# Optimization experiments

Measured on AMD Instinct MI355X. Metric: run time of the kernel, lower is better.

Reference implementation:

```python
import jax, jax.numpy as jnp
import numpy as np

N, E, F_IN, H, H2, G, C = 30000, 480000, 1280, 512, 256, 64, 10


def _linear_init(key, fan_in, fan_out):
    k1, k2 = jax.random.split(key)
    s = 1.0 / np.sqrt(fan_in)
    W = jax.random.uniform(k1, (fan_in, fan_out), jnp.float32, -s, s)
    b = jax.random.uniform(k2, (fan_out,), jnp.float32, -s, s)
    return W, b


def setup_inputs() -> dict:
    key = jax.random.key(0)
    ks = jax.random.split(key, 6)
    x = jax.random.normal(ks[0], (N, F_IN), jnp.float32)
    edge_index = jax.random.randint(ks[1], (2, E), 0, N, dtype=jnp.int32).astype(jnp.int64)
    batch = jnp.sort(jax.random.randint(ks[2], (N,), 0, G, dtype=jnp.int32)).astype(jnp.int64)
    W1, b1 = _linear_init(ks[3], F_IN, H)
    beta2 = jnp.ones((), jnp.float32)  # AGNNConv beta init = 1.0 (trainable in prop2)
    W2, b2 = _linear_init(ks[4], H, H2)
    W3, b3 = _linear_init(ks[5], 2 * H2, C)
    return {"x": x, "edge_index": edge_index, "batch": batch,
            "W1": W1, "b1": b1, "beta2": beta2,
            "W2": W2, "b2": b2, "W3": W3, "b3": b3}


def _agnn(x, src, dst, beta, n):
    # L2 normalize (PyG F.normalize: clamp norm at 1e-12)
    norm = jnp.maximum(jnp.linalg.norm(x, axis=-1, keepdims=True), 1e-12)
    xn = x / norm
    # per-edge cosine similarity attention logits
    alpha = beta * jnp.sum(xn[src] * xn[dst], axis=-1)  # [E']
    # softmax over incoming edges of each destination node
    amax = jax.ops.segment_max(alpha, dst, num_segments=n)
    ex = jnp.exp(alpha - amax[dst])
    denom = jax.ops.segment_sum(ex, dst, num_segments=n)
    w = ex / denom[dst]
    # weighted scatter-add of raw source features
    return jax.ops.segment_sum(w[:, None] * x[src], dst, num_segments=n)


def reference(x, edge_index, batch, W1, b1, beta2, W2, b2, W3, b3):
    n = x.shape[0]
    h = jax.nn.relu(x @ W1 + b1)  # [N, 512]
    # AGNNConv adds self-loops by default
    loops = jnp.arange(n, dtype=edge_index.dtype)
    src = jnp.concatenate([edge_index[0], loops])
    dst = jnp.concatenate([edge_index[1], loops])
    h = _agnn(h, src, dst, jnp.float32(1.0), n)  # prop1: fixed beta=1
    h = _agnn(h, src, dst, beta2, n)             # prop2: learned beta
    h = jax.nn.relu(h @ W2 + b2)  # [N, 256]
    # global max / mean pool per graph
    gmx = jax.ops.segment_max(h, batch, num_segments=G)
    cnt = jnp.maximum(jax.ops.segment_sum(jnp.ones((n,), h.dtype), batch, num_segments=G), 1.0)
    gav = jax.ops.segment_sum(h, batch, num_segments=G) / cnt[:, None]
    return jnp.concatenate([gmx, gav], axis=1) @ W3 + b3  # [G, C]
```

## Files before the change

### kernel.cpp

```cpp
#include <hip/hip_runtime.h>
#include <hip/hip_bf16.h>
#include <cstdint>


typedef __attribute__((ext_vector_type(8))) short bf16x8;
typedef __attribute__((ext_vector_type(4))) float f32x4;
typedef __attribute__((ext_vector_type(8))) unsigned short ushort8;
typedef __attribute__((ext_vector_type(4))) unsigned short ushort4v;
typedef __attribute__((ext_vector_type(4))) unsigned int uint4v;

__device__ inline unsigned short f2bf(float f) {
    unsigned int u = __float_as_uint(f);
    u += 0x7FFFu + ((u >> 16) & 1u);
    return (unsigned short)(u >> 16);
}

__device__ __forceinline__ float bf2f(unsigned short u) {
    return __uint_as_float(((unsigned int)u) << 16);
}

__device__ __forceinline__ unsigned int cvtpk(float lo, float hi) {
    unsigned int r;
    asm("v_cvt_pk_bf16_f32 %0, %1, %2" : "=v"(r) : "v"(lo), "v"(hi));
    return r;
}

__device__ __forceinline__ void gload_lds16(const void* g, void* l) {
    __builtin_amdgcn_global_load_lds(
        (const __attribute__((address_space(1))) void*)g,
        (__attribute__((address_space(3))) void*)l, 16, 0, 0);
}

__device__ __forceinline__ float wave_sum_dpp(float p) {
    int t;
    t = __builtin_amdgcn_update_dpp(0, __float_as_int(p), 0xB1, 0xf, 0xf, true);
    p += __int_as_float(t);
    t = __builtin_amdgcn_update_dpp(0, __float_as_int(p), 0x4E, 0xf, 0xf, true);
    p += __int_as_float(t);
    t = __builtin_amdgcn_update_dpp(0, __float_as_int(p), 0x141, 0xf, 0xf, true);
    p += __int_as_float(t);
    t = __builtin_amdgcn_update_dpp(0, __float_as_int(p), 0x140, 0xf, 0xf, true);
    p += __int_as_float(t);
    t = __builtin_amdgcn_update_dpp(0, __float_as_int(p), 0x142, 0xf, 0xf, true);
    p += __int_as_float(t);
    t = __builtin_amdgcn_update_dpp(0, __float_as_int(p), 0x143, 0xf, 0xf, true);
    p += __int_as_float(t);
    return __int_as_float(__builtin_amdgcn_readlane(__float_as_int(p), 63));
}

__global__ __launch_bounds__(256) void k_transpose_bf16(
    const float* __restrict__ W, unsigned short* __restrict__ Wt, int K, int N) {
    __shared__ unsigned short t[32][33];
    int k0 = blockIdx.x * 32, n0 = blockIdx.y * 32;
    int tr = threadIdx.x >> 3;
    int tc = (threadIdx.x & 7) * 4;
    float4 v = *(const float4*)(W + (long)(k0 + tr) * N + n0 + tc);
    t[tr][tc + 0] = f2bf(v.x); t[tr][tc + 1] = f2bf(v.y);
    t[tr][tc + 2] = f2bf(v.z); t[tr][tc + 3] = f2bf(v.w);
    __syncthreads();
    ushort4v o = { t[tc + 0][tr], t[tc + 1][tr], t[tc + 2][tr], t[tc + 3][tr] };
    *(ushort4v*)(Wt + (long)(n0 + tr) * K + k0 + tc) = o;
}

template <int K, int BN, int NOUT, bool AF32, bool OUTBF16>
__global__ __launch_bounds__(512, 4) void k_gemm_bias_relu(
    const void* __restrict__ Av, const unsigned short* __restrict__ Bt,
    const float* __restrict__ bias, void* __restrict__ Cv, int M) {
    constexpr int NSTEP = K / 32;
    __shared__ unsigned short As[2][128 * 32];
    __shared__ unsigned short Bs[2][BN * 32];
    int tid = threadIdx.x;
    int w = tid >> 6, l = tid & 63;
    int wm = w >> 2, wn = w & 3;
    int mBase = blockIdx.x * 128;
    int nBase = blockIdx.y * BN;

    const float* Af = (const float*)Av;
    const unsigned short* Ab = (const unsigned short*)Av;

    int arow = tid >> 2;
    int aslot = (tid & 3) ^ ((arow >> 1) & 3);
    long aRowG = mBase + arow; if (aRowG >= M) aRowG = M - 1;
    const float* aptr = AF32 ? (Af + aRowG * K + (tid & 3) * 8) : nullptr;

    auto stageB = [&](int b, int k0) {
#pragma unroll
        for (int o = 0; o < BN / 128; ++o) {
            int rbase = (w * (BN / 128) + o) * 16;
            int row = rbase + (l >> 2);
            int gsrc = (l & 3) ^ ((row >> 1) & 3);
            gload_lds16(Bt + (long)(nBase + row) * K + k0 + gsrc * 8,
                        &Bs[b][rbase * 32]);
        }
    };
    auto stageAbf = [&](int b, int k0) {
        int rbase = w * 16;
        int row = rbase + (l >> 2);
        int gsrc = (l & 3) ^ ((row >> 1) & 3);
        long gr = mBase + row; if (gr >= M) gr = M - 1;
        gload_lds16(Ab + gr * K + k0 + gsrc * 8, &As[b][rbase * 32]);
    };

    f32x4 acc[4][4] = {};
    float4 Aw0 = {}, Aw1 = {}, An0 = {}, An1 = {};

    stageB(0, 0);
    if constexpr (AF32) {
        float4 z0 = *(const float4*)(aptr);
        float4 z1 = *(const float4*)(aptr + 4);
        uint4v p = { cvtpk(z0.x, z0.y), cvtpk(z0.z, z0.w),
                     cvtpk(z1.x, z1.y), cvtpk(z1.z, z1.w) };
        *(uint4v*)(&As[0][arow * 32 + aslot * 8]) = p;
        if (NSTEP > 1) {
            Aw0 = *(const float4*)(aptr + 32);
            Aw1 = *(const float4*)(aptr + 36);
        }
    } else {
        stageAbf(0, 0);
    }
    __syncthreads();

    int s = 0;
    for (int step = 0; step < NSTEP; ++step, s ^= 1) {
        int nk = (step + 1) * 32;
        int nk2 = (step + 2) * 32;
        if (nk < K) {
            stageB(s ^ 1, nk);
            if constexpr (!AF32) stageAbf(s ^ 1, nk);
        }
        if constexpr (AF32) {
            if (nk2 < K) {
                An0 = *(const float4*)(aptr + nk2);
                An1 = *(const float4*)(aptr + nk2 + 4);
            }
        }
        bf16x8 af[4];
#pragma unroll
        for (int m = 0; m < 4; ++m) {
            int ra = wm * 64 + m * 16 + (l & 15);
            int g = (l >> 4) ^ ((ra >> 1) & 3);
            af[m] = *(const bf16x8*)(&As[s][ra * 32 + g * 8]);
        }
#pragma unroll
        for (int n = 0; n < 4; ++n) {
            int rb = wn * 64 + n * 16 + (l & 15);
            int g = (l >> 4) ^ ((rb >> 1) & 3);
            bf16x8 bfr = *(const bf16x8*)(&Bs[s][rb * 32 + g * 8]);
#pragma unroll
            for (int m = 0; m < 4; ++m)
                acc[m][n] = __builtin_amdgcn_mfma_f32_16x16x32_bf16(
                    af[m], bfr, acc[m][n], 0, 0, 0);
        }
        if constexpr (AF32) {
            if (nk < K) {
                uint4v p = { cvtpk(Aw0.x, Aw0.y), cvtpk(Aw0.z, Aw0.w),
                             cvtpk(Aw1.x, Aw1.y), cvtpk(Aw1.z, Aw1.w) };
                *(uint4v*)(&As[s ^ 1][arow * 32 + aslot * 8]) = p;
                Aw0 = An0; Aw1 = An1;
            }
        }
        __syncthreads();
    }

#pragma unroll
    for (int m = 0; m < 4; ++m) {
        int row = mBase + wm * 64 + m * 16 + (l >> 4) * 4;
#pragma unroll
        for (int n = 0; n < 4; ++n) {
            int colg = nBase + wn * 64 + n * 16 + (l & 15);
            float bv = bias[colg];
#pragma unroll
            for (int r = 0; r < 4; ++r) {
                if (row + r < M) {
                    float v = fmaxf(acc[m][n][r] + bv, 0.f);
                    if constexpr (OUTBF16)
                        ((unsigned short*)Cv)[(long)(row + r) * NOUT + colg] = f2bf(v);
                    else
                        ((float*)Cv)[(long)(row + r) * NOUT + colg] = v;
                }
            }
        }
    }
}

__global__ void k_csr_init(int* __restrict__ cnt, int* __restrict__ fill, int n) {
    int i = blockIdx.x * blockDim.x + threadIdx.x;
    if (i < n) { cnt[i] = 1; fill[i] = 0; }
}

__global__ void k_csr_count(const int* __restrict__ ei, int* __restrict__ cnt, int E) {
    int e = blockIdx.x * blockDim.x + threadIdx.x;
    if (e < E) atomicAdd(&cnt[ei[E + e]], 1);
}

__global__ __launch_bounds__(1024) void k_scan1(const int* __restrict__ cnt,
                                                int* __restrict__ rowp,
                                                int* __restrict__ bsum, int n) {
    __shared__ int wsum[16];
    int b = blockIdx.x, t = threadIdx.x, lane = t & 63, w = t >> 6;
    int i = b * 1024 + t;
    int v = (i < n) ? cnt[i] : 0;
    int x = v;
#pragma unroll
    for (int off = 1; off < 64; off <<= 1) {
        int y = __shfl_up(x, off, 64);
        if (lane >= off) x += y;
    }
    if (lane == 63) wsum[w] = x;
    __syncthreads();
    if (t < 16) {
        int s = wsum[t];
#pragma unroll
        for (int off = 1; off < 16; off <<= 1) {
            int y = __shfl_up(s, off, 64);
            if (t >= off) s += y;
        }
        wsum[t] = s;
    }
    __syncthreads();
    int wo = w ? wsum[w - 1] : 0;
    if (i < n) rowp[i] = wo + x - v;
    if (t == 0) bsum[b] = wsum[15];
}

__global__ __launch_bounds__(64) void k_scan2(int* __restrict__ bsum, int nb) {
    int lane = threadIdx.x;
    int v = (lane < nb) ? bsum[lane] : 0;
    int x = v;
#pragma unroll
    for (int off = 1; off < 64; off <<= 1) {
        int y = __shfl_up(x, off, 64);
        if (lane >= off) x += y;
    }
    int total = __shfl(x, nb - 1, 64);
    if (lane < nb) bsum[lane] = x - v;
    if (lane == 0) bsum[nb] = total;
}

__global__ __launch_bounds__(1024) void k_scan3(const int* __restrict__ bsum,
                                                int* __restrict__ rowp, int n, int nb) {
    int i = blockIdx.x * 1024 + threadIdx.x;
    if (i < n) rowp[i] += bsum[i >> 10];
    else if (i == n) rowp[n] = bsum[nb];
}

__global__ void k_csr_fill(const int* __restrict__ ei, const int* __restrict__ rowp,
                           int* __restrict__ fill, int* __restrict__ col, int E, int n) {
    int idx = blockIdx.x * blockDim.x + threadIdx.x;
    if (idx < E) {
        int d = ei[E + idx];
        int s = ei[idx];
        int pos = atomicAdd(&fill[d], 1);
        col[rowp[d] + pos] = s;
    } else if (idx < E + n) {
        int nd = idx - E;
        int pos = atomicAdd(&fill[nd], 1);
        col[rowp[nd] + pos] = nd;
    }
}

__global__ __launch_bounds__(256) void k_norm_bf16(const unsigned short* __restrict__ h,
                                                   float* __restrict__ invn, int n) {
    int row = blockIdx.x * 4 + (threadIdx.x >> 6);
    int lane = threadIdx.x & 63;
    if (row >= n) return;
    ushort8 v = *(const ushort8*)(h + (long)row * 512 + lane * 8);
    float s = 0.f;
#pragma unroll
    for (int e = 0; e < 8; ++e) { float f = bf2f(v[e]); s += f * f; }
    s = wave_sum_dpp(s);
    if (lane == 0) invn[row] = 1.f / fmaxf(sqrtf(s), 1e-12f);
}

__global__ __launch_bounds__(256) void k_agnn(
    const unsigned short* __restrict__ h, const float* __restrict__ invn,
    const int* __restrict__ rowp, const int* __restrict__ col,
    const float* __restrict__ beta_ptr, unsigned short* __restrict__ out,
    float* __restrict__ invn_out, int nNodes) {
    int dst = blockIdx.x * 4 + (threadIdx.x >> 6);
    int lane = threadIdx.x & 63;
    if (dst >= nNodes) return;
    float beta = beta_ptr ? beta_ptr[0] : 1.0f;
    ushort8 hdv = *(const ushort8*)(h + (long)dst * 512 + lane * 8);
    float hd[8];
#pragma unroll
    for (int e = 0; e < 8; ++e) hd[e] = bf2f(hdv[e]);
    float coef = beta * invn[dst];
    float mshift = fabsf(beta) * 1.0625f;
    int s0 = rowp[dst], s1 = rowp[dst + 1];

    float ssum = 0.f;
    float accE[8] = {0.f, 0.f, 0.f, 0.f, 0.f, 0.f, 0.f, 0.f};
    float accO[8] = {0.f, 0.f, 0.f, 0.f, 0.f, 0.f, 0.f, 0.f};

    for (int base = s0; base < s1; base += 64) {
        int cnt = min(s1 - base, 64);
        int gi = base + lane; if (gi >= s1) gi = s1 - 1;
        int idxl = col[gi];
        float vinl = invn[idxl];
        ushort8 r0 = {}, r1 = {}, r2 = {}, r3 = {};
        r0 = *(const ushort8*)(h + (long)__builtin_amdgcn_readlane(idxl, 0) * 512 + lane * 8);
        if (cnt > 1) r1 = *(const ushort8*)(h + (long)__builtin_amdgcn_readlane(idxl, 1) * 512 + lane * 8);
        if (cnt > 2) r2 = *(const ushort8*)(h + (long)__builtin_amdgcn_readlane(idxl, 2) * 512 + lane * 8);
        if (cnt > 3) r3 = *(const ushort8*)(h + (long)__builtin_amdgcn_readlane(idxl, 3) * 512 + lane * 8);
        int j = 0;
        for (; j + 1 < cnt; j += 2) {
            ushort8 c0 = r0, c1 = r1;
            r0 = r2; r1 = r3;
            if (j + 4 < cnt) r2 = *(const ushort8*)(h + (long)__builtin_amdgcn_readlane(idxl, j + 4) * 512 + lane * 8);
            if (j + 5 < cnt) r3 = *(const ushort8*)(h + (long)__builtin_amdgcn_readlane(idxl, j + 5) * 512 + lane * 8);
            float a0[8], a1[8];
#pragma unroll
            for (int e = 0; e < 8; ++e) { a0[e] = bf2f(c0[e]); a1[e] = bf2f(c1[e]); }
            float p0 = a0[0] * hd[0] + a0[1] * hd[1] + a0[2] * hd[2] + a0[3] * hd[3] +
                       a0[4] * hd[4] + a0[5] * hd[5] + a0[6] * hd[6] + a0[7] * hd[7];
            float p1 = a1[0] * hd[0] + a1[1] * hd[1] + a1[2] * hd[2] + a1[3] * hd[3] +
                       a1[4] * hd[4] + a1[5] * hd[5] + a1[6] * hd[6] + a1[7] * hd[7];
            p0 = wave_sum_dpp(p0);
            p1 = wave_sum_dpp(p1);
            float al0 = coef * __int_as_float(__builtin_amdgcn_readlane(__float_as_int(vinl), j)) * p0;
            float al1 = coef * __int_as_float(__builtin_amdgcn_readlane(__float_as_int(vinl), j + 1)) * p1;
            float w0 = __expf(al0 - mshift);
            float w1 = __expf(al1 - mshift);
            ssum += w0 + w1;
#pragma unroll
            for (int e = 0; e < 8; ++e) { accE[e] += w0 * a0[e]; accO[e] += w1 * a1[e]; }
        }
        if (j < cnt) {
            float a0[8];
#pragma unroll
            for (int e = 0; e < 8; ++e) a0[e] = bf2f(r0[e]);
            float p0 = a0[0] * hd[0] + a0[1] * hd[1] + a0[2] * hd[2] + a0[3] * hd[3] +
                       a0[4] * hd[4] + a0[5] * hd[5] + a0[6] * hd[6] + a0[7] * hd[7];
            p0 = wave_sum_dpp(p0);
            float al0 = coef * __int_as_float(__builtin_amdgcn_readlane(__float_as_int(vinl), j)) * p0;
            float w0 = __expf(al0 - mshift);
            ssum += w0;
#pragma unroll
            for (int e = 0; e < 8; ++e) accE[e] += w0 * a0[e];
        }
    }
    float inv_s = 1.f / ssum;
    float acc[8];
#pragma unroll
    for (int e = 0; e < 8; ++e) acc[e] = (accE[e] + accO[e]) * inv_s;

    uint4v o = { cvtpk(acc[0], acc[1]), cvtpk(acc[2], acc[3]),
                 cvtpk(acc[4], acc[5]), cvtpk(acc[6], acc[7]) };
    *(uint4v*)(out + (long)dst * 512 + lane * 8) = o;

    if (invn_out) {
        float s = 0.f;
#pragma unroll
        for (int e = 0; e < 8; ++e) s += acc[e] * acc[e];
        s = wave_sum_dpp(s);
        if (lane == 0) invn_out[dst] = 1.f / fmaxf(sqrtf(s), 1e-12f);
    }
}

__global__ void k_bounds(const int* __restrict__ batch, int* __restrict__ starts,
                         int n, int G) {
    int g = blockIdx.x * blockDim.x + threadIdx.x;
    if (g > G) return;
    int lo = 0, hi = n;
    while (lo < hi) {
        int mid = (lo + hi) >> 1;
        if (batch[mid] < g) lo = mid + 1; else hi = mid;
    }
    starts[g] = lo;
}

__global__ __launch_bounds__(256) void k_pool(const float* __restrict__ h3,
                                              const int* __restrict__ starts,
                                              float* __restrict__ pooled) {
    int g = blockIdx.x;
    int t = threadIdx.x;
    int s = starts[g], e = starts[g + 1];
    float mx = -3.402823466e38f, sm = 0.f;
    int r = s;
    for (; r + 4 <= e; r += 4) {
        float v0 = h3[(long)(r + 0) * 256 + t];
        float v1 = h3[(long)(r + 1) * 256 + t];
        float v2 = h3[(long)(r + 2) * 256 + t];
        float v3 = h3[(long)(r + 3) * 256 + t];
        mx = fmaxf(mx, fmaxf(fmaxf(v0, v1), fmaxf(v2, v3)));
        sm += (v0 + v1) + (v2 + v3);
    }
    for (; r < e; ++r) {
        float v = h3[(long)r * 256 + t];
        mx = fmaxf(mx, v); sm += v;
    }
    float cnt = fmaxf((float)(e - s), 1.f);
    pooled[g * 512 + t] = mx;
    pooled[g * 512 + 256 + t] = sm / cnt;
}

__global__ __launch_bounds__(64) void k_final(const float* __restrict__ pooled,
                                              const float* __restrict__ W3,
                                              const float* __restrict__ b3,
                                              float* __restrict__ out, int C) {
    int g = blockIdx.x;
    int lane = threadIdx.x;
    for (int c = 0; c < C; c++) {
        float p = 0.f;
        for (int k = lane; k < 512; k += 64) p += pooled[g * 512 + k] * W3[k * C + c];
#pragma unroll
        for (int off = 32; off; off >>= 1) p += __shfl_xor(p, off, 64);
        if (lane == 0) out[g * C + c] = p + b3[c];
    }
}

extern "C" void kernel_launch(void* const* d_in, const int* in_sizes, int n_in,
                              void* d_out, int out_size, void* d_ws, size_t ws_size,
                              hipStream_t stream) {
    const float* x     = (const float*)d_in[0];
    const int*   ei    = (const int*)d_in[1];
    const int*   batch = (const int*)d_in[2];
    const float* W1    = (const float*)d_in[3];
    const float* b1    = (const float*)d_in[4];
    const float* beta2 = (const float*)d_in[5];
    const float* W2    = (const float*)d_in[6];
    const float* b2    = (const float*)d_in[7];
    const float* W3    = (const float*)d_in[8];
    const float* b3    = (const float*)d_in[9];
    float* out = (float*)d_out;

    const int N = in_sizes[2];
    const int E = in_sizes[1] / 2;
    const int F_IN = in_sizes[0] / N;
    const int H = in_sizes[4];
    const int H2 = in_sizes[7];
    const int C = in_sizes[9];
    const int G = out_size / C;

    char* ws = (char*)d_ws;
    unsigned short* H1B = (unsigned short*)(ws + 0);
    unsigned short* HPB = (unsigned short*)(ws + 31000000L);
    unsigned short* H2B = (unsigned short*)(ws + 62000000L);
    float*          H3  = (float*)(ws + 0);
    unsigned short* W1T = (unsigned short*)(ws + 93000000L);
    unsigned short* W2T = (unsigned short*)(ws + 94500000L);
    float* INVN_A = (float*)(ws + 95000000L);
    float* INVN_B = (float*)(ws + 95200000L);
    int*   CNT    = (int*)(ws + 95400000L);
    int*   FILL   = (int*)(ws + 95600000L);
    int*   ROWP   = (int*)(ws + 95800000L);
    int*   COL    = (int*)(ws + 96000000L);
    int*   BSUM   = (int*)(ws + 98100000L);
    int*   START  = (int*)(ws + 98110000L);
    float* POOLED = (float*)(ws + 98120000L);

    { dim3 g1(F_IN / 32, H / 32); k_transpose_bf16<<<g1, 256, 0, stream>>>(W1, W1T, F_IN, H); }
    { dim3 g2(H / 32, H2 / 32);   k_transpose_bf16<<<g2, 256, 0, stream>>>(W2, W2T, H, H2); }

    int nb = (N + 1023) / 1024;
    k_csr_init<<<(N + 255) / 256, 256, 0, stream>>>(CNT, FILL, N);
    k_csr_count<<<(E + 255) / 256, 256, 0, stream>>>(ei, CNT, E);
    k_scan1<<<nb, 1024, 0, stream>>>(CNT, ROWP, BSUM, N);
    k_scan2<<<1, 64, 0, stream>>>(BSUM, nb);
    k_scan3<<<(N + 1 + 1023) / 1024, 1024, 0, stream>>>(BSUM, ROWP, N, nb);
    k_csr_fill<<<(E + N + 255) / 256, 256, 0, stream>>>(ei, ROWP, FILL, COL, E, N);

    {
        dim3 grid((N + 127) / 128, H / 256);
        k_gemm_bias_relu<1280, 256, 512, true, true>
            <<<grid, 512, 0, stream>>>(x, W1T, b1, H1B, N);
    }

    k_norm_bf16<<<(N + 3) / 4, 256, 0, stream>>>(H1B, INVN_A, N);
    k_agnn<<<(N + 3) / 4, 256, 0, stream>>>(H1B, INVN_A, ROWP, COL, nullptr, HPB, INVN_B, N);

    k_agnn<<<(N + 3) / 4, 256, 0, stream>>>(HPB, INVN_B, ROWP, COL, beta2, H2B, nullptr, N);

    {
        dim3 grid((N + 127) / 128, 1);
        k_gemm_bias_relu<512, 256, 256, false, false>
            <<<grid, 512, 0, stream>>>(H2B, W2T, b2, H3, N);
    }

    k_bounds<<<1, 128, 0, stream>>>(batch, START, N, G);
    k_pool<<<G, 256, 0, stream>>>(H3, START, POOLED);
    k_final<<<G, 64, 0, stream>>>(POOLED, W3, b3, out, C);
}
```

Measured before the change: 379.3 us.

## Merge small launches, shrink GEMM2 tile, emit bf16 H3, and simplify A prefetch

Fuses the two weight-transpose kernels into one launch, merges scan2 and scan3 into one kernel, and folds the batch-bounds search into the pooling kernel, which cuts three launches. The second GEMM now uses BN=128 with two column blocks, so it launches more workgroups, and it writes its output as bf16 to halve the bytes the pooling kernel reads. The fp32 A prefetch in the first GEMM now runs one step ahead instead of two, which may expose more load latency. Storing H3 as bf16 adds rounding error before pooling.

```diff
diff --git a/kernel.cpp b/kernel.cpp
--- a/kernel.cpp
+++ b/kernel.cpp
@@ -48,17 +48,30 @@
     return __int_as_float(__builtin_amdgcn_readlane(__float_as_int(p), 63));
 }
 
-__global__ __launch_bounds__(256) void k_transpose_bf16(
-    const float* __restrict__ W, unsigned short* __restrict__ Wt, int K, int N) {
-    __shared__ unsigned short t[32][33];
-    int k0 = blockIdx.x * 32, n0 = blockIdx.y * 32;
+__global__ __launch_bounds__(256) void k_transpose_both(
+    const float* __restrict__ W1, unsigned short* __restrict__ W1T,
+    int K1, int N1, int nt1,
+    const float* __restrict__ W2, unsigned short* __restrict__ W2T,
+    int K2, int N2) {
+    __shared__ unsigned short tb[32][33];
+    int id = blockIdx.x;
+    const float* W; unsigned short* Wt; int K, N, bx, by;
+    if (id < nt1) {
+        W = W1; Wt = W1T; K = K1; N = N1;
+        int nx = K1 / 32; bx = id % nx; by = id / nx;
+    } else {
+        id -= nt1;
+        W = W2; Wt = W2T; K = K2; N = N2;
+        int nx = K2 / 32; bx = id % nx; by = id / nx;
+    }
+    int k0 = bx * 32, n0 = by * 32;
     int tr = threadIdx.x >> 3;
     int tc = (threadIdx.x & 7) * 4;
     float4 v = *(const float4*)(W + (long)(k0 + tr) * N + n0 + tc);
-    t[tr][tc + 0] = f2bf(v.x); t[tr][tc + 1] = f2bf(v.y);
-    t[tr][tc + 2] = f2bf(v.z); t[tr][tc + 3] = f2bf(v.w);
-    __syncthreads();
-    ushort4v o = { t[tc + 0][tr], t[tc + 1][tr], t[tc + 2][tr], t[tc + 3][tr] };
+    tb[tr][tc + 0] = f2bf(v.x); tb[tr][tc + 1] = f2bf(v.y);
+    tb[tr][tc + 2] = f2bf(v.z); tb[tr][tc + 3] = f2bf(v.w);
+    __syncthreads();
+    ushort4v o = { tb[tc + 0][tr], tb[tc + 1][tr], tb[tc + 2][tr], tb[tc + 3][tr] };
     *(ushort4v*)(Wt + (long)(n0 + tr) * K + k0 + tc) = o;
 }
 
@@ -67,6 +80,7 @@
     const void* __restrict__ Av, const unsigned short* __restrict__ Bt,
     const float* __restrict__ bias, void* __restrict__ Cv, int M) {
     constexpr int NSTEP = K / 32;
+    constexpr int NF = BN / 64;
     __shared__ unsigned short As[2][128 * 32];
     __shared__ unsigned short Bs[2][BN * 32];
     int tid = threadIdx.x;
@@ -101,8 +115,7 @@
         gload_lds16(Ab + gr * K + k0 + gsrc * 8, &As[b][rbase * 32]);
     };
 
-    f32x4 acc[4][4] = {};
-    float4 Aw0 = {}, Aw1 = {}, An0 = {}, An1 = {};
+    f32x4 acc[4][NF] = {};
 
     stageB(0, 0);
     if constexpr (AF32) {
@@ -111,10 +124,6 @@
         uint4v p = { cvtpk(z0.x, z0.y), cvtpk(z0.z, z0.w),
                      cvtpk(z1.x, z1.y), cvtpk(z1.z, z1.w) };
         *(uint4v*)(&As[0][arow * 32 + aslot * 8]) = p;
-        if (NSTEP > 1) {
-            Aw0 = *(const float4*)(aptr + 32);
-            Aw1 = *(const float4*)(aptr + 36);
-        }
     } else {
         stageAbf(0, 0);
     }
@@ -123,15 +132,14 @@
     int s = 0;
     for (int step = 0; step < NSTEP; ++step, s ^= 1) {
         int nk = (step + 1) * 32;
-        int nk2 = (step + 2) * 32;
+        float4 f0, f1;
         if (nk < K) {
             stageB(s ^ 1, nk);
-            if constexpr (!AF32) stageAbf(s ^ 1, nk);
-        }
-        if constexpr (AF32) {
-            if (nk2 < K) {
-                An0 = *(const float4*)(aptr + nk2);
-                An1 = *(const float4*)(aptr + nk2 + 4);
+            if constexpr (AF32) {
+                f0 = *(const float4*)(aptr + nk);
+                f1 = *(const float4*)(aptr + nk + 4);
+            } else {
+                stageAbf(s ^ 1, nk);
             }
         }
         bf16x8 af[4];
@@ -142,8 +150,8 @@
             af[m] = *(const bf16x8*)(&As[s][ra * 32 + g * 8]);
         }
 #pragma unroll
-        for (int n = 0; n < 4; ++n) {
-            int rb = wn * 64 + n * 16 + (l & 15);
+        for (int n = 0; n < NF; ++n) {
+            int rb = wn * (BN / 4) + n * 16 + (l & 15);
             int g = (l >> 4) ^ ((rb >> 1) & 3);
             bf16x8 bfr = *(const bf16x8*)(&Bs[s][rb * 32 + g * 8]);
 #pragma unroll
@@ -153,10 +161,9 @@
         }
         if constexpr (AF32) {
             if (nk < K) {
-                uint4v p = { cvtpk(Aw0.x, Aw0.y), cvtpk(Aw0.z, Aw0.w),
-                             cvtpk(Aw1.x, Aw1.y), cvtpk(Aw1.z, Aw1.w) };
+                uint4v p = { cvtpk(f0.x, f0.y), cvtpk(f0.z, f0.w),
+                             cvtpk(f1.x, f1.y), cvtpk(f1.z, f1.w) };
                 *(uint4v*)(&As[s ^ 1][arow * 32 + aslot * 8]) = p;
-                Aw0 = An0; Aw1 = An1;
             }
         }
         __syncthreads();
@@ -166,8 +173,8 @@
     for (int m = 0; m < 4; ++m) {
         int row = mBase + wm * 64 + m * 16 + (l >> 4) * 4;
 #pragma unroll
-        for (int n = 0; n < 4; ++n) {
-            int colg = nBase + wn * 64 + n * 16 + (l & 15);
+        for (int n = 0; n < NF; ++n) {
+            int colg = nBase + wn * (BN / 4) + n * 16 + (l & 15);
             float bv = bias[colg];
 #pragma unroll
             for (int r = 0; r < 4; ++r) {
@@ -223,25 +230,25 @@
     if (t == 0) bsum[b] = wsum[15];
 }
 
-__global__ __launch_bounds__(64) void k_scan2(int* __restrict__ bsum, int nb) {
-    int lane = threadIdx.x;
-    int v = (lane < nb) ? bsum[lane] : 0;
-    int x = v;
-#pragma unroll
-    for (int off = 1; off < 64; off <<= 1) {
-        int y = __shfl_up(x, off, 64);
-        if (lane >= off) x += y;
-    }
-    int total = __shfl(x, nb - 1, 64);
-    if (lane < nb) bsum[lane] = x - v;
-    if (lane == 0) bsum[nb] = total;
-}
-
-__global__ __launch_bounds__(1024) void k_scan3(const int* __restrict__ bsum,
-                                                int* __restrict__ rowp, int n, int nb) {
-    int i = blockIdx.x * 1024 + threadIdx.x;
-    if (i < n) rowp[i] += bsum[i >> 10];
-    else if (i == n) rowp[n] = bsum[nb];
+__global__ __launch_bounds__(1024) void k_scan23(const int* __restrict__ bsum,
+                                                 int* __restrict__ rowp, int n, int nb) {
+    __shared__ int off[65];
+    int t = threadIdx.x;
+    if (t < 64) {
+        int v = (t < nb) ? bsum[t] : 0;
+        int x = v;
+#pragma unroll
+        for (int o = 1; o < 64; o <<= 1) {
+            int y = __shfl_up(x, o, 64);
+            if (t >= o) x += y;
+        }
+        off[t] = x - v;
+        if (t == nb - 1) off[64] = x;
+    }
+    __syncthreads();
+    int i = blockIdx.x * 1024 + t;
+    if (i < n) rowp[i] += off[i >> 10];
+    else if (i == n) rowp[n] = off[64];
 }
 
 __global__ void k_csr_fill(const int* __restrict__ ei, const int* __restrict__ rowp,
@@ -358,36 +365,35 @@
     }
 }
 
-__global__ void k_bounds(const int* __restrict__ batch, int* __restrict__ starts,
-                         int n, int G) {
-    int g = blockIdx.x * blockDim.x + threadIdx.x;
-    if (g > G) return;
-    int lo = 0, hi = n;
-    while (lo < hi) {
-        int mid = (lo + hi) >> 1;
-        if (batch[mid] < g) lo = mid + 1; else hi = mid;
-    }
-    starts[g] = lo;
-}
-
-__global__ __launch_bounds__(256) void k_pool(const float* __restrict__ h3,
-                                              const int* __restrict__ starts,
-                                              float* __restrict__ pooled) {
+__global__ __launch_bounds__(256) void k_pool(const unsigned short* __restrict__ h3,
+                                              const int* __restrict__ batch,
+                                              float* __restrict__ pooled, int n) {
+    __shared__ int se[2];
     int g = blockIdx.x;
+    if (threadIdx.x < 2) {
+        int tgt = g + (int)threadIdx.x;
+        int lo = 0, hi = n;
+        while (lo < hi) {
+            int mid = (lo + hi) >> 1;
+            if (batch[mid] < tgt) lo = mid + 1; else hi = mid;
+        }
+        se[threadIdx.x] = lo;
+    }
+    __syncthreads();
+    int s = se[0], e = se[1];
     int t = threadIdx.x;
-    int s = starts[g], e = starts[g + 1];
     float mx = -3.402823466e38f, sm = 0.f;
     int r = s;
     for (; r + 4 <= e; r += 4) {
-        float v0 = h3[(long)(r + 0) * 256 + t];
-        float v1 = h3[(long)(r + 1) * 256 + t];
-        float v2 = h3[(long)(r + 2) * 256 + t];
-        float v3 = h3[(long)(r + 3) * 256 + t];
+        float v0 = bf2f(h3[(long)(r + 0) * 256 + t]);
+        float v1 = bf2f(h3[(long)(r + 1) * 256 + t]);
+        float v2 = bf2f(h3[(long)(r + 2) * 256 + t]);
+        float v3 = bf2f(h3[(long)(r + 3) * 256 + t]);
         mx = fmaxf(mx, fmaxf(fmaxf(v0, v1), fmaxf(v2, v3)));
         sm += (v0 + v1) + (v2 + v3);
     }
     for (; r < e; ++r) {
-        float v = h3[(long)r * 256 + t];
+        float v = bf2f(h3[(long)r * 256 + t]);
         mx = fmaxf(mx, v); sm += v;
     }
     float cnt = fmaxf((float)(e - s), 1.f);
@@ -435,9 +441,9 @@
 
     char* ws = (char*)d_ws;
     unsigned short* H1B = (unsigned short*)(ws + 0);
+    unsigned short* H3B = (unsigned short*)(ws + 0);
     unsigned short* HPB = (unsigned short*)(ws + 31000000L);
     unsigned short* H2B = (unsigned short*)(ws + 62000000L);
-    float*          H3  = (float*)(ws + 0);
     unsigned short* W1T = (unsigned short*)(ws + 93000000L);
     unsigned short* W2T = (unsigned short*)(ws + 94500000L);
     float* INVN_A = (float*)(ws + 95000000L);
@@ -447,18 +453,18 @@
     int*   ROWP   = (int*)(ws + 95800000L);
     int*   COL    = (int*)(ws + 96000000L);
     int*   BSUM   = (int*)(ws + 98100000L);
-    int*   START  = (int*)(ws + 98110000L);
     float* POOLED = (float*)(ws + 98120000L);
 
-    { dim3 g1(F_IN / 32, H / 32); k_transpose_bf16<<<g1, 256, 0, stream>>>(W1, W1T, F_IN, H); }
-    { dim3 g2(H / 32, H2 / 32);   k_transpose_bf16<<<g2, 256, 0, stream>>>(W2, W2T, H, H2); }
+    int nt1 = (F_IN / 32) * (H / 32);
+    int nt2 = (H / 32) * (H2 / 32);
+    k_transpose_both<<<nt1 + nt2, 256, 0, stream>>>(W1, W1T, F_IN, H, nt1,
+                                                    W2, W2T, H, H2);
 
     int nb = (N + 1023) / 1024;
     k_csr_init<<<(N + 255) / 256, 256, 0, stream>>>(CNT, FILL, N);
     k_csr_count<<<(E + 255) / 256, 256, 0, stream>>>(ei, CNT, E);
     k_scan1<<<nb, 1024, 0, stream>>>(CNT, ROWP, BSUM, N);
-    k_scan2<<<1, 64, 0, stream>>>(BSUM, nb);
-    k_scan3<<<(N + 1 + 1023) / 1024, 1024, 0, stream>>>(BSUM, ROWP, N, nb);
+    k_scan23<<<(N + 1 + 1023) / 1024, 1024, 0, stream>>>(BSUM, ROWP, N, nb);
     k_csr_fill<<<(E + N + 255) / 256, 256, 0, stream>>>(ei, ROWP, FILL, COL, E, N);
 
     {
@@ -473,12 +479,11 @@
     k_agnn<<<(N + 3) / 4, 256, 0, stream>>>(HPB, INVN_B, ROWP, COL, beta2, H2B, nullptr, N);
 
     {
-        dim3 grid((N + 127) / 128, 1);
-        k_gemm_bias_relu<512, 256, 256, false, false>
-            <<<grid, 512, 0, stream>>>(H2B, W2T, b2, H3, N);
-    }
-
-    k_bounds<<<1, 128, 0, stream>>>(batch, START, N, G);
-    k_pool<<<G, 256, 0, stream>>>(H3, START, POOLED);
+        dim3 grid((N + 127) / 128, H2 / 128);
+        k_gemm_bias_relu<512, 128, 256, false, true>
+            <<<grid, 512, 0, stream>>>(H2B, W2T, b2, H3B, N);
+    }
+
+    k_pool<<<G, 256, 0, stream>>>(H3B, batch, POOLED, N);
     k_final<<<G, 64, 0, stream>>>(POOLED, W3, b3, out, C);
 }
```

After: 353.1 us. 6.9% less time.
